# Kernel tuning notes

Hardware: AMD Instinct MI355X
Metric: run time of the kernel (lower is better)

The kernel has to match this reference:

```python
import jax, jax.numpy as jnp
import numpy as np

D = 256   # vec_dim
H = 8     # head_num
P = 1024  # patch_num
N = 8     # batch


def setup_inputs() -> dict:
    key = jax.random.key(0)
    ks = jax.random.split(key, 11)
    s = 0.05
    return {
        "inputs": jax.random.normal(ks[0], (N, D, P), dtype=jnp.float32),
        "pos_mat": jax.random.normal(ks[1], (1, H, P, P), dtype=jnp.float32),
        "Wk": jax.random.normal(ks[2], (H * D, D), dtype=jnp.float32) * s,
        "bk": jax.random.normal(ks[3], (H * D,), dtype=jnp.float32) * s,
        "Wq": jax.random.normal(ks[4], (H * D, D), dtype=jnp.float32) * s,
        "bq": jax.random.normal(ks[5], (H * D,), dtype=jnp.float32) * s,
        "Wv": jax.random.normal(ks[6], (H * D, D), dtype=jnp.float32) * s,
        "bv": jax.random.normal(ks[7], (H * D,), dtype=jnp.float32) * s,
        "Wo": jax.random.normal(ks[8], (D, H * D), dtype=jnp.float32) * s,
        "bo": jax.random.normal(ks[9], (D,), dtype=jnp.float32) * s,
    }


def reference(inputs, pos_mat, Wk, bk, Wq, bq, Wv, bv, Wo, bo):
    n, d, p = inputs.shape  # [N, D, P]
    h = Wk.shape[0] // d
    # 1x1 Conv1d == per-position GEMM: [H*D,D] x [N,D,P] -> [N,H*D,P] -> [N,H,D,P]
    k = (jnp.einsum('od,ndp->nop', Wk, inputs) + bk[:, None]).reshape(n, h, d, p)
    q = (jnp.einsum('od,ndp->nop', Wq, inputs) + bq[:, None]).reshape(n, h, d, p)
    v = (jnp.einsum('od,ndp->nop', Wv, inputs) + bv[:, None]).reshape(n, h, d, p)
    # attn[n,h,kpos,qpos] = K^T Q / sqrt(D), shape [N,H,P,P]
    attn = jnp.einsum('nhdk,nhdq->nhkq', k, q) / jnp.sqrt(jnp.asarray(d, inputs.dtype))
    attn = attn + pos_mat
    # NOTE: original uses Softmax(dim=2), i.e. over the KEY axis, not the last dim
    w = jax.nn.softmax(attn, axis=2)
    out = jnp.einsum('nhdk,nhkq->nhdq', v, w).reshape(n, h * d, p)
    return jnp.einsum('oi,nip->nop', Wo, out) + bo[:, None]
```

## Files before the change

kernel.cpp:

```cpp
#include <hip/hip_runtime.h>

typedef __bf16 bf16;
typedef __attribute__((ext_vector_type(8))) __bf16 bf16x8;
typedef __attribute__((ext_vector_type(4))) __bf16 bf16x4;
typedef __attribute__((ext_vector_type(2))) __bf16 bf16x2;
typedef __attribute__((ext_vector_type(4))) float f32x4;

#define MFMA16(a, b, c) __builtin_amdgcn_mfma_f32_16x16x32_bf16(a, b, c, 0, 0, 0)

constexpr int NH = 8, DD = 256, PP = 1024;

constexpr size_t WB_YT  = 33554432;
constexpr size_t WB_XB  = 67108864;
constexpr size_t WB_XBT = 71303168;
constexpr size_t WB_MB  = 75497472;
constexpr size_t WB_UB  = 76546048;
constexpr size_t WB_U   = 77594624;
constexpr size_t WB_BP  = 77602816;

constexpr int FL_PT   = 0;
constexpr int FL_LRED = 8192;
constexpr int FL_XT   = 32768;
constexpr int FL_SZ   = 65536;

#define EXP_SHIFT 4.0f

__global__ __launch_bounds__(256, 1) void msa_mu(
    const float* __restrict__ Wk, const float* __restrict__ Wq,
    const float* __restrict__ Wo, const float* __restrict__ Wv,
    bf16* __restrict__ Mb, bf16* __restrict__ Ub) {
  __shared__ float lds[64 * 65];
  const int t = threadIdx.x;
  const int i0 = (blockIdx.x >> 1) * 64;
  const int jh = blockIdx.x & 1;
  const int h = blockIdx.y;
  const int mode = blockIdx.z;
  const int j0 = (t & 63) * 2 + jh * 128;
  const int ihalf = t >> 6;
  float acc0[16], acc1[16];
#pragma unroll
  for (int r = 0; r < 16; ++r) { acc0[r] = 0.f; acc1[r] = 0.f; }
  const float* __restrict__ W2 = (mode == 0) ? Wq : Wv;
  for (int dhc = 0; dhc < 256; dhc += 64) {
    __syncthreads();
    if (mode == 0) {
#pragma unroll
      for (int s = 0; s < 16; ++s) {
        int f = t + s * 256;
        int dh = f >> 6, ii = f & 63;
        lds[dh * 65 + ii] = Wk[(h * 256 + dhc + dh) * 256 + i0 + ii];
      }
    } else {
#pragma unroll
      for (int s = 0; s < 16; ++s) {
        int f = t + s * 256;
        int oo = f >> 6, dh = f & 63;
        lds[dh * 65 + oo] = Wo[(i0 + oo) * 2048 + h * 256 + dhc + dh];
      }
    }
    __syncthreads();
    for (int dl = 0; dl < 64; ++dl) {
      float2 wv = *reinterpret_cast<const float2*>(&W2[(h * 256 + dhc + dl) * 256 + j0]);
#pragma unroll
      for (int r = 0; r < 16; ++r) {
        float x = lds[dl * 65 + ihalf * 16 + r];
        acc0[r] = fmaf(x, wv.x, acc0[r]);
        acc1[r] = fmaf(x, wv.y, acc1[r]);
      }
    }
  }
  if (mode == 0) {
#pragma unroll
    for (int r = 0; r < 16; ++r) {
      int i = i0 + ihalf * 16 + r;
      bf16x2 v = { (__bf16)(acc0[r] * 0.0625f), (__bf16)(acc1[r] * 0.0625f) };
      *reinterpret_cast<bf16x2*>(&Mb[h * 65536 + i * 256 + j0]) = v;
    }
  } else {
#pragma unroll
    for (int r = 0; r < 16; ++r) {
      int o = i0 + ihalf * 16 + r;
      bf16x2 v = { (__bf16)acc0[r], (__bf16)acc1[r] };
      *reinterpret_cast<bf16x2*>(&Ub[o * 2048 + h * 256 + j0]) = v;
    }
  }
}

__global__ void msa_u(const float* __restrict__ Wk, const float* __restrict__ bq,
                      float* __restrict__ u) {
  __shared__ float bqs[256];
  const int h = blockIdx.x, t = threadIdx.x;
  bqs[t] = bq[h * 256 + t];
  __syncthreads();
  float acc = 0.f;
  for (int dh = 0; dh < 256; ++dh)
    acc = fmaf(Wk[(h * 256 + dh) * 256 + t], bqs[dh], acc);
  u[h * 256 + t] = acc * 0.0625f;
}

__global__ void msa_bp(const float* __restrict__ Wo, const float* __restrict__ bv,
                       const float* __restrict__ bo, float* __restrict__ bp) {
  const int o = blockIdx.x, t = threadIdx.x;
  float acc = 0.f;
  for (int f = t; f < 2048; f += 256)
    acc = fmaf(Wo[o * 2048 + f], bv[f], acc);
#pragma unroll
  for (int m = 32; m >= 1; m >>= 1) acc += __shfl_down(acc, m);
  __shared__ float part[4];
  if ((t & 63) == 0) part[t >> 6] = acc;
  __syncthreads();
  if (t == 0) bp[o] = bo[o] + part[0] + part[1] + part[2] + part[3];
}

__global__ __launch_bounds__(256, 4) void msa_cvtX(
    const float* __restrict__ X, bf16* __restrict__ Xb, bf16* __restrict__ XbT) {
  __shared__ __bf16 tl[64 * 68];
  const int t = threadIdx.x;
  const int p0 = blockIdx.x * 64, d0 = blockIdx.y * 64, n = blockIdx.z;
  const float* __restrict__ Xn = X + (size_t)n * DD * PP;
#pragma unroll
  for (int rr = 0; rr < 4; ++rr) {
    int r = (t >> 4) + rr * 16, c = (t & 15) * 4;
    float4 v = *reinterpret_cast<const float4*>(Xn + (size_t)(d0 + r) * PP + p0 + c);
    bf16x4 pk = { (__bf16)v.x, (__bf16)v.y, (__bf16)v.z, (__bf16)v.w };
    *reinterpret_cast<bf16x4*>(Xb + (size_t)n * DD * PP + (size_t)(d0 + r) * PP + p0 + c) = pk;
    *reinterpret_cast<bf16x4*>(&tl[r * 68 + c]) = pk;
  }
  __syncthreads();
#pragma unroll
  for (int rr = 0; rr < 4; ++rr) {
    int pr = (t >> 4) + rr * 16, dc = (t & 15) * 4;
    bf16x4 pk = { tl[(dc + 0) * 68 + pr], tl[(dc + 1) * 68 + pr],
                  tl[(dc + 2) * 68 + pr], tl[(dc + 3) * 68 + pr] };
    *reinterpret_cast<bf16x4*>(XbT + (size_t)n * PP * DD + (size_t)(p0 + pr) * DD + d0 + dc) = pk;
  }
}

__global__ __launch_bounds__(256, 2) void msa_flash(
    const bf16* __restrict__ XbT, const bf16* __restrict__ Xb,
    const bf16* __restrict__ Mb, const float* __restrict__ u,
    const float* __restrict__ pos, bf16* __restrict__ Yt) {
  extern __shared__ char smc[];
  const int t = threadIdx.x;
  const int lane = t & 63, w = t >> 6;
  const int g = lane >> 4, ln = lane & 15;
  const int kw = w >> 1, qw = w & 1;
  const int qt = blockIdx.x, h = blockIdx.y, n = blockIdx.z;
  const int qg0 = qt * 64, nh = n * 8 + h;
  const bf16* __restrict__ XbTn = XbT + (size_t)n * (PP * DD);
  const bf16* __restrict__ Xbn  = Xb + (size_t)n * (DD * PP);
  const bf16* __restrict__ Mh   = Mb + (size_t)h * (DD * DD);
  const float* __restrict__ posh = pos + (size_t)h * (PP * PP);
  float* lredp = (float*)(smc + FL_LRED);

  {
    bf16x8 ta[4][8];
#pragma unroll
    for (int mq = 0; mq < 4; ++mq)
#pragma unroll
      for (int s = 0; s < 8; ++s)
        ta[mq][s] = *reinterpret_cast<const bf16x8*>(
            XbTn + (size_t)(qg0 + mq * 16 + ln) * DD + s * 32 + g * 8);
#pragma unroll
    for (int ni = 0; ni < 4; ++ni) {
      const int i_ = w * 64 + ni * 16 + ln;
      bf16x8 tb8[8];
#pragma unroll
      for (int s = 0; s < 8; ++s)
        tb8[s] = *reinterpret_cast<const bf16x8*>(Mh + (size_t)i_ * DD + s * 32 + g * 8);
      const float uv = u[h * 256 + i_];
#pragma unroll
      for (int mq = 0; mq < 4; ++mq) {
        f32x4 acc = {0.f, 0.f, 0.f, 0.f};
#pragma unroll
        for (int s = 0; s < 8; ++s) acc = MFMA16(ta[mq][s], tb8[s], acc);
#pragma unroll
        for (int r = 0; r < 4; ++r) {
          const int q = mq * 16 + 4 * g + r;
          const int addr = q * 512 +
              (((w * 8 + ni * 2 + (ln >> 3)) ^ (q & 7)) << 4) + (ln & 7) * 2;
          *reinterpret_cast<__bf16*>(smc + addr) = (__bf16)(acc[r] + uv);
        }
      }
    }
  }
  __syncthreads();

  bf16x8 tb[2][8];
#pragma unroll
  for (int nq = 0; nq < 2; ++nq) {
    const int q_ = qw * 32 + nq * 16 + ln;
#pragma unroll
    for (int s = 0; s < 8; ++s)
      tb[nq][s] = *reinterpret_cast<const bf16x8*>(
          smc + q_ * 512 + (((4 * s + g) ^ (q_ & 7)) << 4));
  }
  __syncthreads();

  float lsum[2] = {0.f, 0.f};
  f32x4 yacc[4][4];
#pragma unroll
  for (int a = 0; a < 4; ++a)
#pragma unroll
    for (int b = 0; b < 4; ++b) { f32x4 z = {0.f, 0.f, 0.f, 0.f}; yacc[a][b] = z; }

  for (int kt = 0; kt < 16; ++kt) {
    const int kg0 = kt * 64;
#pragma unroll
    for (int c = 0; c < 8; ++c) {
      int flat = t + c * 256;
      int row = flat >> 5, cb = flat & 31;
      uint4 v = *reinterpret_cast<const uint4*>(XbTn + (size_t)(kg0 + row) * DD + cb * 8);
      *reinterpret_cast<uint4*>(smc + FL_XT + row * 512 + ((cb ^ (row & 7)) << 4)) = v;
    }
    float posv[2][2][4];
#pragma unroll
    for (int mt = 0; mt < 2; ++mt)
#pragma unroll
      for (int nq = 0; nq < 2; ++nq) {
        const float* pr = posh + (size_t)(kg0 + kw * 32 + mt * 16 + 4 * g) * PP +
                          qg0 + qw * 32 + nq * 16 + ln;
#pragma unroll
        for (int r = 0; r < 4; ++r) posv[mt][nq][r] = pr[(size_t)r * PP];
      }
    __syncthreads();

    f32x4 sacc[2][2];
#pragma unroll
    for (int a = 0; a < 2; ++a)
#pragma unroll
      for (int b = 0; b < 2; ++b) { f32x4 z = {0.f, 0.f, 0.f, 0.f}; sacc[a][b] = z; }
#pragma unroll
    for (int mt = 0; mt < 2; ++mt) {
      const int row = kw * 32 + mt * 16 + ln;
      bf16x8 af8[8];
#pragma unroll
      for (int s = 0; s < 8; ++s)
        af8[s] = *reinterpret_cast<const bf16x8*>(
            smc + FL_XT + row * 512 + (((4 * s + g) ^ (row & 7)) << 4));
#pragma unroll
      for (int s = 0; s < 8; ++s)
#pragma unroll
        for (int nq = 0; nq < 2; ++nq)
          sacc[mt][nq] = MFMA16(af8[s], tb[nq][s], sacc[mt][nq]);
    }
#pragma unroll
    for (int mt = 0; mt < 2; ++mt)
#pragma unroll
      for (int nq = 0; nq < 2; ++nq) {
        bf16x4 pk;
#pragma unroll
        for (int r = 0; r < 4; ++r) {
          float e = __expf(sacc[mt][nq][r] + posv[mt][nq][r] - EXP_SHIFT);
          lsum[nq] += e;
          pk[r] = (__bf16)e;
        }
        const int q_ = qw * 32 + nq * 16 + ln;
        *reinterpret_cast<bf16x4*>(smc + FL_PT + q_ * 128 +
            (((kw * 4 + mt * 2 + (g >> 1)) ^ (q_ & 7)) << 4) + ((g & 1) << 3)) = pk;
      }
    __syncthreads();

#pragma unroll
    for (int ks = 0; ks < 2; ++ks) {
      bf16x8 pa[4], xv[4];
#pragma unroll
      for (int mq = 0; mq < 4; ++mq) {
        const int q_ = mq * 16 + ln;
        pa[mq] = *reinterpret_cast<const bf16x8*>(
            smc + FL_PT + q_ * 128 + (((4 * ks + g) ^ (q_ & 7)) << 4));
      }
#pragma unroll
      for (int nd = 0; nd < 4; ++nd)
        xv[nd] = *reinterpret_cast<const bf16x8*>(
            Xbn + (size_t)(w * 64 + nd * 16 + ln) * PP + kg0 + ks * 32 + g * 8);
#pragma unroll
      for (int mq = 0; mq < 4; ++mq)
#pragma unroll
        for (int nd = 0; nd < 4; ++nd)
          yacc[mq][nd] = MFMA16(pa[mq], xv[nd], yacc[mq][nd]);
    }
  }

#pragma unroll
  for (int nq = 0; nq < 2; ++nq) {
    lsum[nq] += __shfl_xor(lsum[nq], 16);
    lsum[nq] += __shfl_xor(lsum[nq], 32);
  }
  if (lane < 16) {
#pragma unroll
    for (int nq = 0; nq < 2; ++nq)
      lredp[kw * 64 + qw * 32 + nq * 16 + ln] = lsum[nq];
  }
  __syncthreads();
  bf16* __restrict__ Ytp = Yt + (size_t)nh * (PP * DD);
#pragma unroll
  for (int mq = 0; mq < 4; ++mq) {
    f32x4 l0 = *reinterpret_cast<const f32x4*>(lredp + mq * 16 + 4 * g);
    f32x4 l1 = *reinterpret_cast<const f32x4*>(lredp + 64 + mq * 16 + 4 * g);
    f32x4 inv;
#pragma unroll
    for (int r = 0; r < 4; ++r) inv[r] = 1.0f / (l0[r] + l1[r]);
#pragma unroll
    for (int nd = 0; nd < 4; ++nd)
#pragma unroll
      for (int r = 0; r < 4; ++r)
        Ytp[(size_t)(qg0 + mq * 16 + 4 * g + r) * DD + w * 64 + nd * 16 + ln] =
            (__bf16)(yacc[mq][nd][r] * inv[r]);
  }
}

__global__ __launch_bounds__(256, 2) void msa_final3(
    const bf16* __restrict__ Ub, const bf16* __restrict__ Yt,
    const float* __restrict__ bp, float* __restrict__ out) {
  const int t = threadIdx.x, lane = t & 63, w = t >> 6;
  const int g = lane >> 4, ln = lane & 15;
  const int pt = blockIdx.x, n = blockIdx.y;
  const bf16* __restrict__ Ytn = Yt + (size_t)n * 8 * (PP * DD);
  f32x4 acc[4][2];
#pragma unroll
  for (int a = 0; a < 4; ++a)
#pragma unroll
    for (int b = 0; b < 2; ++b) { f32x4 z = {0.f, 0.f, 0.f, 0.f}; acc[a][b] = z; }
#pragma unroll 4
  for (int js = 0; js < 64; ++js) {
    const int hh = js >> 3, dd = (js & 7) * 32;
    bf16x8 a[4], b[2];
#pragma unroll
    for (int mo = 0; mo < 4; ++mo)
      a[mo] = *reinterpret_cast<const bf16x8*>(
          Ub + (size_t)(w * 64 + mo * 16 + ln) * 2048 + js * 32 + g * 8);
#pragma unroll
    for (int np = 0; np < 2; ++np)
      b[np] = *reinterpret_cast<const bf16x8*>(
          Ytn + ((size_t)hh * PP + pt * 32 + np * 16 + ln) * DD + dd + g * 8);
#pragma unroll
    for (int mo = 0; mo < 4; ++mo)
#pragma unroll
      for (int np = 0; np < 2; ++np) acc[mo][np] = MFMA16(a[mo], b[np], acc[mo][np]);
  }
#pragma unroll
  for (int mo = 0; mo < 4; ++mo) {
    f32x4 bv = *reinterpret_cast<const f32x4*>(bp + w * 64 + mo * 16 + 4 * g);
#pragma unroll
    for (int np = 0; np < 2; ++np)
#pragma unroll
      for (int r = 0; r < 4; ++r) {
        const int o = w * 64 + mo * 16 + 4 * g + r;
        out[((size_t)n * DD + o) * PP + pt * 32 + np * 16 + ln] = acc[mo][np][r] + bv[r];
      }
  }
}

extern "C" void kernel_launch(void* const* d_in, const int* in_sizes, int n_in,
                              void* d_out, int out_size, void* d_ws, size_t ws_size,
                              hipStream_t stream) {
  const float* X   = (const float*)d_in[0];
  const float* pos = (const float*)d_in[1];
  const float* Wk  = (const float*)d_in[2];
  const float* Wq  = (const float*)d_in[4];
  const float* bq  = (const float*)d_in[5];
  const float* Wv  = (const float*)d_in[6];
  const float* bv  = (const float*)d_in[7];
  const float* Wo  = (const float*)d_in[8];
  const float* bo  = (const float*)d_in[9];

  char* ws = (char*)d_ws;
  bf16* Yt  = (bf16*)(ws + WB_YT);
  bf16* Xb  = (bf16*)(ws + WB_XB);
  bf16* XbT = (bf16*)(ws + WB_XBT);
  bf16* Mb  = (bf16*)(ws + WB_MB);
  bf16* Ub  = (bf16*)(ws + WB_UB);
  float* u  = (float*)(ws + WB_U);
  float* bp = (float*)(ws + WB_BP);
  float* out = (float*)d_out;

  hipFuncSetAttribute(reinterpret_cast<const void*>(msa_flash),
                      hipFuncAttributeMaxDynamicSharedMemorySize, FL_SZ);

  msa_cvtX<<<dim3(16, 4, 8), 256, 0, stream>>>(X, Xb, XbT);
  msa_mu<<<dim3(8, 8, 2), 256, 0, stream>>>(Wk, Wq, Wo, Wv, Mb, Ub);
  msa_u<<<8, 256, 0, stream>>>(Wk, bq, u);
  msa_bp<<<256, 256, 0, stream>>>(Wo, bv, bo, bp);
  msa_flash<<<dim3(16, 8, 8), 256, FL_SZ, stream>>>(XbT, Xb, Mb, u, pos, Yt);
  msa_final3<<<dim3(32, 8), 256, 0, stream>>>(Ub, Yt, bp, out);
}
```

Measured before the change: 312.4 us.

## Software-pipeline flash loop with double-buffered LDS and retile final projection

The flash kernel now double-buffers the key tile and the probability tile in LDS. It prefetches the next key tile and pos values into registers and runs the P·V MFMAs one iteration behind, which cuts the syncs per iteration from two to one. The final output projection is rewritten as an LDS-staged, double-buffered GEMM with 64x128 tiles and a 3D grid, replacing the direct global-load version. The cost is more LDS (80KB for flash) and more registers, which may limit occupancy.

New measurement: 376.8 us. 20.6% more time.

```diff
diff --git a/kernel.cpp b/kernel.cpp
--- a/kernel.cpp
+++ b/kernel.cpp
@@ -18,10 +18,10 @@
 constexpr size_t WB_U   = 77594624;
 constexpr size_t WB_BP  = 77602816;
 
-constexpr int FL_PT   = 0;
-constexpr int FL_LRED = 8192;
-constexpr int FL_XT   = 32768;
-constexpr int FL_SZ   = 65536;
+constexpr int FL_PT0  = 0;
+constexpr int FL_XT0  = 16384;
+constexpr int FL_LRED = 16384;
+constexpr int FL_SZ   = 81920;
 
 #define EXP_SHIFT 4.0f
 
@@ -177,7 +177,7 @@
 #pragma unroll
         for (int r = 0; r < 4; ++r) {
           const int q = mq * 16 + 4 * g + r;
-          const int addr = q * 512 +
+          const int addr = FL_XT0 + q * 512 +
               (((w * 8 + ni * 2 + (ln >> 3)) ^ (q & 7)) << 4) + (ln & 7) * 2;
           *reinterpret_cast<__bf16*>(smc + addr) = (__bf16)(acc[r] + uv);
         }
@@ -193,7 +193,32 @@
 #pragma unroll
     for (int s = 0; s < 8; ++s)
       tb[nq][s] = *reinterpret_cast<const bf16x8*>(
-          smc + q_ * 512 + (((4 * s + g) ^ (q_ & 7)) << 4));
+          smc + FL_XT0 + q_ * 512 + (((4 * s + g) ^ (q_ & 7)) << 4));
+  }
+  __syncthreads();
+
+  uint4 xreg[8];
+#pragma unroll
+  for (int c = 0; c < 8; ++c) {
+    int flat = t + c * 256;
+    int row = flat >> 5, cb = flat & 31;
+    xreg[c] = *reinterpret_cast<const uint4*>(XbTn + (size_t)row * DD + cb * 8);
+  }
+  float posv[2][2][4];
+#pragma unroll
+  for (int mt = 0; mt < 2; ++mt)
+#pragma unroll
+    for (int nq = 0; nq < 2; ++nq) {
+      const float* pr = posh + (size_t)(kw * 32 + mt * 16 + 4 * g) * PP +
+                        qg0 + qw * 32 + nq * 16 + ln;
+#pragma unroll
+      for (int r = 0; r < 4; ++r) posv[mt][nq][r] = pr[(size_t)r * PP];
+    }
+#pragma unroll
+  for (int c = 0; c < 8; ++c) {
+    int flat = t + c * 256;
+    int row = flat >> 5, cb = flat & 31;
+    *reinterpret_cast<uint4*>(smc + FL_XT0 + row * 512 + ((cb ^ (row & 7)) << 4)) = xreg[c];
   }
   __syncthreads();
 
@@ -206,25 +231,28 @@
 
   for (int kt = 0; kt < 16; ++kt) {
     const int kg0 = kt * 64;
-#pragma unroll
-    for (int c = 0; c < 8; ++c) {
-      int flat = t + c * 256;
-      int row = flat >> 5, cb = flat & 31;
-      uint4 v = *reinterpret_cast<const uint4*>(XbTn + (size_t)(kg0 + row) * DD + cb * 8);
-      *reinterpret_cast<uint4*>(smc + FL_XT + row * 512 + ((cb ^ (row & 7)) << 4)) = v;
-    }
-    float posv[2][2][4];
-#pragma unroll
-    for (int mt = 0; mt < 2; ++mt)
-#pragma unroll
-      for (int nq = 0; nq < 2; ++nq) {
-        const float* pr = posh + (size_t)(kg0 + kw * 32 + mt * 16 + 4 * g) * PP +
-                          qg0 + qw * 32 + nq * 16 + ln;
-#pragma unroll
-        for (int r = 0; r < 4; ++r) posv[mt][nq][r] = pr[(size_t)r * PP];
-      }
-    __syncthreads();
-
+    const int curXT = FL_XT0 + (kt & 1) * 32768;
+    const int nxtXT = FL_XT0 + ((kt + 1) & 1) * 32768;
+    const int curPT = FL_PT0 + (kt & 1) * 8192;
+    const int prvPT = FL_PT0 + ((kt + 1) & 1) * 8192;
+    if (kt < 15) {
+#pragma unroll
+      for (int c = 0; c < 8; ++c) {
+        int flat = t + c * 256;
+        int row = flat >> 5, cb = flat & 31;
+        xreg[c] = *reinterpret_cast<const uint4*>(
+            XbTn + (size_t)(kg0 + 64 + row) * DD + cb * 8);
+      }
+    }
+    bf16x8 xv[2][4];
+    if (kt > 0) {
+#pragma unroll
+      for (int ks = 0; ks < 2; ++ks)
+#pragma unroll
+        for (int nd = 0; nd < 4; ++nd)
+          xv[ks][nd] = *reinterpret_cast<const bf16x8*>(
+              Xbn + (size_t)(w * 64 + nd * 16 + ln) * PP + (kg0 - 64) + ks * 32 + g * 8);
+    }
     f32x4 sacc[2][2];
 #pragma unroll
     for (int a = 0; a < 2; ++a)
@@ -237,7 +265,7 @@
 #pragma unroll
       for (int s = 0; s < 8; ++s)
         af8[s] = *reinterpret_cast<const bf16x8*>(
-            smc + FL_XT + row * 512 + (((4 * s + g) ^ (row & 7)) << 4));
+            smc + curXT + row * 512 + (((4 * s + g) ^ (row & 7)) << 4));
 #pragma unroll
       for (int s = 0; s < 8; ++s)
 #pragma unroll
@@ -256,29 +284,68 @@
           pk[r] = (__bf16)e;
         }
         const int q_ = qw * 32 + nq * 16 + ln;
-        *reinterpret_cast<bf16x4*>(smc + FL_PT + q_ * 128 +
+        *reinterpret_cast<bf16x4*>(smc + curPT + q_ * 128 +
             (((kw * 4 + mt * 2 + (g >> 1)) ^ (q_ & 7)) << 4) + ((g & 1) << 3)) = pk;
       }
+    if (kt < 15) {
+#pragma unroll
+      for (int mt = 0; mt < 2; ++mt)
+#pragma unroll
+        for (int nq = 0; nq < 2; ++nq) {
+          const float* pr = posh + (size_t)(kg0 + 64 + kw * 32 + mt * 16 + 4 * g) * PP +
+                            qg0 + qw * 32 + nq * 16 + ln;
+#pragma unroll
+          for (int r = 0; r < 4; ++r) posv[mt][nq][r] = pr[(size_t)r * PP];
+        }
+    }
+    if (kt > 0) {
+#pragma unroll
+      for (int ks = 0; ks < 2; ++ks) {
+        bf16x8 pa[4];
+#pragma unroll
+        for (int mq = 0; mq < 4; ++mq) {
+          const int q_ = mq * 16 + ln;
+          pa[mq] = *reinterpret_cast<const bf16x8*>(
+              smc + prvPT + q_ * 128 + (((4 * ks + g) ^ (q_ & 7)) << 4));
+        }
+#pragma unroll
+        for (int mq = 0; mq < 4; ++mq)
+#pragma unroll
+          for (int nd = 0; nd < 4; ++nd)
+            yacc[mq][nd] = MFMA16(pa[mq], xv[ks][nd], yacc[mq][nd]);
+      }
+    }
+    if (kt < 15) {
+#pragma unroll
+      for (int c = 0; c < 8; ++c) {
+        int flat = t + c * 256;
+        int row = flat >> 5, cb = flat & 31;
+        *reinterpret_cast<uint4*>(smc + nxtXT + row * 512 + ((cb ^ (row & 7)) << 4)) = xreg[c];
+      }
+    }
     __syncthreads();
-
+  }
+
+  {
+    const int kg0 = 15 * 64;
 #pragma unroll
     for (int ks = 0; ks < 2; ++ks) {
-      bf16x8 pa[4], xv[4];
+      bf16x8 pa[4], xv2[4];
 #pragma unroll
       for (int mq = 0; mq < 4; ++mq) {
         const int q_ = mq * 16 + ln;
         pa[mq] = *reinterpret_cast<const bf16x8*>(
-            smc + FL_PT + q_ * 128 + (((4 * ks + g) ^ (q_ & 7)) << 4));
+            smc + FL_PT0 + 8192 + q_ * 128 + (((4 * ks + g) ^ (q_ & 7)) << 4));
       }
 #pragma unroll
       for (int nd = 0; nd < 4; ++nd)
-        xv[nd] = *reinterpret_cast<const bf16x8*>(
+        xv2[nd] = *reinterpret_cast<const bf16x8*>(
             Xbn + (size_t)(w * 64 + nd * 16 + ln) * PP + kg0 + ks * 32 + g * 8);
 #pragma unroll
       for (int mq = 0; mq < 4; ++mq)
 #pragma unroll
         for (int nd = 0; nd < 4; ++nd)
-          yacc[mq][nd] = MFMA16(pa[mq], xv[nd], yacc[mq][nd]);
+          yacc[mq][nd] = MFMA16(pa[mq], xv2[nd], yacc[mq][nd]);
     }
   }
 
@@ -310,44 +377,111 @@
   }
 }
 
-__global__ __launch_bounds__(256, 2) void msa_final3(
+__global__ __launch_bounds__(256, 3) void msa_final4(
     const bf16* __restrict__ Ub, const bf16* __restrict__ Yt,
     const float* __restrict__ bp, float* __restrict__ out) {
+  __shared__ char lsd[49152];
   const int t = threadIdx.x, lane = t & 63, w = t >> 6;
   const int g = lane >> 4, ln = lane & 15;
-  const int pt = blockIdx.x, n = blockIdx.y;
+  const int pw = w & 1, ow = w >> 1;
+  const int pb = blockIdx.x * 128, ob = blockIdx.y * 64, n = blockIdx.z;
   const bf16* __restrict__ Ytn = Yt + (size_t)n * 8 * (PP * DD);
-  f32x4 acc[4][2];
-#pragma unroll
-  for (int a = 0; a < 4; ++a)
-#pragma unroll
-    for (int b = 0; b < 2; ++b) { f32x4 z = {0.f, 0.f, 0.f, 0.f}; acc[a][b] = z; }
-#pragma unroll 4
-  for (int js = 0; js < 64; ++js) {
-    const int hh = js >> 3, dd = (js & 7) * 32;
-    bf16x8 a[4], b[2];
-#pragma unroll
-    for (int mo = 0; mo < 4; ++mo)
-      a[mo] = *reinterpret_cast<const bf16x8*>(
-          Ub + (size_t)(w * 64 + mo * 16 + ln) * 2048 + js * 32 + g * 8);
-#pragma unroll
-    for (int np = 0; np < 2; ++np)
-      b[np] = *reinterpret_cast<const bf16x8*>(
-          Ytn + ((size_t)hh * PP + pt * 32 + np * 16 + ln) * DD + dd + g * 8);
-#pragma unroll
-    for (int mo = 0; mo < 4; ++mo)
-#pragma unroll
-      for (int np = 0; np < 2; ++np) acc[mo][np] = MFMA16(a[mo], b[np], acc[mo][np]);
-  }
-#pragma unroll
-  for (int mo = 0; mo < 4; ++mo) {
-    f32x4 bv = *reinterpret_cast<const f32x4*>(bp + w * 64 + mo * 16 + 4 * g);
-#pragma unroll
-    for (int np = 0; np < 2; ++np)
+  f32x4 acc[2][4];
+#pragma unroll
+  for (int a = 0; a < 2; ++a)
+#pragma unroll
+    for (int b = 0; b < 4; ++b) { f32x4 z = {0.f, 0.f, 0.f, 0.f}; acc[a][b] = z; }
+
+  uint4 areg[2], breg[4];
+  {
+#pragma unroll
+    for (int j = 0; j < 2; ++j) {
+      int u_ = t + j * 256;
+      areg[j] = *reinterpret_cast<const uint4*>(
+          Ub + (size_t)(ob + (u_ >> 3)) * 2048 + 0 + (u_ & 7) * 8);
+    }
+#pragma unroll
+    for (int j = 0; j < 4; ++j) {
+      int v_ = t + j * 256;
+      breg[j] = *reinterpret_cast<const uint4*>(
+          Ytn + ((size_t)0 * PP + pb + (v_ >> 3)) * DD + 0 + (v_ & 7) * 8);
+    }
+#pragma unroll
+    for (int j = 0; j < 2; ++j) {
+      int u_ = t + j * 256, row = u_ >> 3, cb = u_ & 7;
+      *reinterpret_cast<uint4*>(lsd + row * 128 + ((cb ^ (row & 7)) << 4)) = areg[j];
+    }
+#pragma unroll
+    for (int j = 0; j < 4; ++j) {
+      int v_ = t + j * 256, row = v_ >> 3, cb = v_ & 7;
+      *reinterpret_cast<uint4*>(lsd + 8192 + row * 128 + ((cb ^ (row & 7)) << 4)) = breg[j];
+    }
+  }
+  __syncthreads();
+
+  for (int kc = 0; kc < 32; ++kc) {
+    const int cur = (kc & 1) * 24576;
+    const int nxt = ((kc + 1) & 1) * 24576;
+    if (kc < 31) {
+      const int k1 = (kc + 1) * 64, hh = k1 >> 8, dd = k1 & 255;
+#pragma unroll
+      for (int j = 0; j < 2; ++j) {
+        int u_ = t + j * 256;
+        areg[j] = *reinterpret_cast<const uint4*>(
+            Ub + (size_t)(ob + (u_ >> 3)) * 2048 + k1 + (u_ & 7) * 8);
+      }
+#pragma unroll
+      for (int j = 0; j < 4; ++j) {
+        int v_ = t + j * 256;
+        breg[j] = *reinterpret_cast<const uint4*>(
+            Ytn + ((size_t)hh * PP + pb + (v_ >> 3)) * DD + dd + (v_ & 7) * 8);
+      }
+    }
+#pragma unroll
+    for (int ks = 0; ks < 2; ++ks) {
+      bf16x8 a[2], b[4];
+#pragma unroll
+      for (int mo = 0; mo < 2; ++mo) {
+        const int row = ow * 32 + mo * 16 + ln;
+        a[mo] = *reinterpret_cast<const bf16x8*>(
+            lsd + cur + row * 128 + (((4 * ks + g) ^ (row & 7)) << 4));
+      }
+#pragma unroll
+      for (int np = 0; np < 4; ++np) {
+        const int row = pw * 64 + np * 16 + ln;
+        b[np] = *reinterpret_cast<const bf16x8*>(
+            lsd + cur + 8192 + row * 128 + (((4 * ks + g) ^ (row & 7)) << 4));
+      }
+#pragma unroll
+      for (int mo = 0; mo < 2; ++mo)
+#pragma unroll
+        for (int np = 0; np < 4; ++np) acc[mo][np] = MFMA16(a[mo], b[np], acc[mo][np]);
+    }
+    if (kc < 31) {
+#pragma unroll
+      for (int j = 0; j < 2; ++j) {
+        int u_ = t + j * 256, row = u_ >> 3, cb = u_ & 7;
+        *reinterpret_cast<uint4*>(lsd + nxt + row * 128 + ((cb ^ (row & 7)) << 4)) = areg[j];
+      }
+#pragma unroll
+      for (int j = 0; j < 4; ++j) {
+        int v_ = t + j * 256, row = v_ >> 3, cb = v_ & 7;
+        *reinterpret_cast<uint4*>(lsd + nxt + 8192 + row * 128 + ((cb ^ (row & 7)) << 4)) = breg[j];
+      }
+    }
+    __syncthreads();
+  }
+
+#pragma unroll
+  for (int mo = 0; mo < 2; ++mo) {
+    f32x4 bv = *reinterpret_cast<const f32x4*>(bp + ob + ow * 32 + mo * 16 + 4 * g);
+#pragma unroll
+    for (int np = 0; np < 4; ++np)
 #pragma unroll
       for (int r = 0; r < 4; ++r) {
-        const int o = w * 64 + mo * 16 + 4 * g + r;
-        out[((size_t)n * DD + o) * PP + pt * 32 + np * 16 + ln] = acc[mo][np][r] + bv[r];
+        const int o = ob + ow * 32 + mo * 16 + 4 * g + r;
+        out[((size_t)n * DD + o) * PP + pb + pw * 64 + np * 16 + ln] =
+            acc[mo][np][r] + bv[r];
       }
   }
 }
@@ -383,5 +517,5 @@
   msa_u<<<8, 256, 0, stream>>>(Wk, bq, u);
   msa_bp<<<256, 256, 0, stream>>>(Wo, bv, bo, bp);
   msa_flash<<<dim3(16, 8, 8), 256, FL_SZ, stream>>>(XbT, Xb, Mb, u, pos, Yt);
-  msa_final3<<<dim3(32, 8), 256, 0, stream>>>(Ub, Yt, bp, out);
-}
+  msa_final4<<<dim3(8, 4, 8), 256, 0, stream>>>(Ub, Yt, bp, out);
+}
```
